# Kernel optimization log

Measured on AMD Instinct MI355X. Metric: run time of the kernel, lower is better.

## Reference

```python
import jax, jax.numpy as jnp
import numpy as np

HEADS = 8

def _conv(x, w, b, stride, pad):
    # x: [B,C,H,W], w: [O,I,kh,kw] (torch OIHW layout)
    y = jax.lax.conv_general_dilated(x, w, (stride, stride), ((pad, pad), (pad, pad)),
                                     dimension_numbers=('NCHW', 'OIHW', 'NCHW'))
    return y + b[None, :, None, None]

def _maxpool2x2(x):
    # returns pooled values and one-hot argmax per 2x2 window (torch first-max tie-break)
    b, c, H, W = x.shape
    win = x.reshape(b, c, H // 2, 2, W // 2, 2).transpose(0, 1, 2, 4, 3, 5).reshape(b, c, H // 2, W // 2, 4)
    am = jnp.argmax(win, axis=-1)
    oh = jax.nn.one_hot(am, 4, dtype=x.dtype)
    pooled = jnp.sum(win * oh, axis=-1)
    return pooled, oh

def _maxunpool2x2(y, oh):
    b, c, h2, w2 = y.shape
    out = y[..., None] * oh  # [b,c,h2,w2,4]
    out = out.reshape(b, c, h2, w2, 2, 2).transpose(0, 1, 2, 4, 3, 5).reshape(b, c, h2 * 2, w2 * 2)
    return out

def _mha2d(x, wq, wk, wv, wo):
    # x: [b,c,h,w]; wq/wk/wv/wo stored as [in,out] so y = x @ W
    b, c, h, w = x.shape
    hw = h * w
    dk = wq.shape[1]
    dh = dk // HEADS
    xt = x.reshape(b, c, hw).transpose(0, 2, 1)  # [b,hw,c]
    def split(y):  # torch: view(b,hw,dh,heads).permute(0,3,1,2)
        return y.reshape(b, hw, dh, HEADS).transpose(0, 3, 1, 2)  # [b,heads,hw,dh]
    q = split(xt @ wq)
    k = split(xt @ wk)
    v = split(xt @ wv)
    scale = jnp.sqrt(jnp.asarray(dh, x.dtype))
    attn = jax.nn.softmax(jnp.einsum('bhqd,bhkd->bhqk', q, k) / scale, axis=-1)
    o = jnp.einsum('bhqk,bhkd->bhqd', attn, v)
    o = o.transpose(0, 2, 3, 1).reshape(b, hw, dk)  # [b,hw,dh,heads] -> merge
    o = o @ wo
    return o.transpose(0, 2, 1).reshape(b, dk, h, w)

def setup_inputs() -> dict:
    key = jax.random.key(0)
    ks = jax.random.split(key, 10)
    B, C, H, W = 16, 256, 64, 64
    s = 0.05
    return {
        'x': jax.random.normal(ks[0], (B, C, H, W), jnp.float32),
        'conv_w': jax.random.normal(ks[1], (C, C, 3, 3), jnp.float32) * s,
        'conv_b': jax.random.normal(ks[2], (C,), jnp.float32) * s,
        'fr_w': jax.random.normal(ks[3], (C, C, 1, 1), jnp.float32) * s,
        'fr_b': jax.random.normal(ks[4], (C,), jnp.float32) * s,
        'wq': jax.random.normal(ks[5], (C, C), jnp.float32) * s,
        'wk': jax.random.normal(ks[6], (C, C), jnp.float32) * s,
        'wv': jax.random.normal(ks[7], (C, C), jnp.float32) * s,
        'wo': jax.random.normal(ks[8], (C, C), jnp.float32) * s,
        'gamma': jax.random.normal(ks[9], (1,), jnp.float32) * 0.1,
    }

def reference(x, conv_w, conv_b, fr_w, fr_b, wq, wk, wv, wo, gamma):
    _x = _conv(x, fr_w, fr_b, 1, 0)          # 1x1 feature reduction
    _x, oh = _maxpool2x2(_x)                 # MaxPool2d(2, return_indices=True)
    _x = _mha2d(_x, wq, wk, wv, wo)          # attention over pooled grid
    _x = _maxunpool2x2(_x, oh)               # MaxUnpool2d(2)
    return _x * jnp.tanh(gamma[0]) + _conv(x, conv_w, conv_b, 1, 1)
```

## Files before the change

### kernel.cpp

```cpp
#include <hip/hip_runtime.h>
#include <hip/hip_bf16.h>
#include <math.h>

#define B 16
#define C 256
#define H 64
#define W 64
#define H2 32
#define W2 32
#define HW2 1024
#define HEADS 8
#define DH 32

typedef unsigned short ushort_t;
using short8 = __attribute__((ext_vector_type(8))) short;
using u16x8  = __attribute__((ext_vector_type(8))) unsigned short;
using f32x4  = __attribute__((ext_vector_type(4))) float;

__device__ inline ushort_t f2bf(float f) {
    __hip_bfloat16 hb = __float2bfloat16(f);
    return *(ushort_t*)&hb;
}
__device__ inline float bf2f(ushort_t u) {
    return __uint_as_float(((unsigned)u) << 16);
}

__device__ __forceinline__ void cp16(const ushort_t* g, ushort_t* l) {
    __builtin_amdgcn_global_load_lds(
        (const __attribute__((address_space(1))) void*)g,
        (__attribute__((address_space(3))) void*)l, 16, 0, 0);
}

#define RSCALE 0.17677669529663687f

__global__ __launch_bounds__(256) void k_prep_wT(const float* __restrict__ cw,
                                                 ushort_t* __restrict__ wbfT) {
    int i = threadIdx.x, o = blockIdx.x;
    const float* src = cw + ((size_t)o * C + i) * 9;
#pragma unroll
    for (int kk = 0; kk < 9; kk++)
        wbfT[((size_t)kk * C + o) * C + i] = f2bf(src[kk]);
}

__global__ __launch_bounds__(256) void k_prep_wx(
    const float* __restrict__ wq, const float* __restrict__ wk,
    const float* __restrict__ wv, const float* __restrict__ wo,
    const float* __restrict__ frw, ushort_t* __restrict__ wqkvT,
    ushort_t* __restrict__ woT, ushort_t* __restrict__ wfr) {
    int op = blockIdx.x, mat = blockIdx.y, t = threadIdx.x;
    if (mat < 3) {
        const float* w = (mat == 0) ? wq : (mat == 1) ? wk : wv;
        int hh = op >> 5, d = op & 31, col = d * 8 + hh;
        wqkvT[(size_t)mat * 65536 + op * 256 + t] = f2bf(w[t * 256 + col]);
    } else if (mat == 3) {
        int hh = t >> 5, d = t & 31, ic = d * 8 + hh;
        woT[op * 256 + t] = f2bf(wo[ic * 256 + op]);
    } else {
        wfr[op * 256 + t] = f2bf(frw[op * 256 + t]);
    }
}

__global__ __launch_bounds__(256) void k_prep_xn(const float* __restrict__ x,
                                                 ushort_t* __restrict__ xn) {
    __shared__ ushort_t ldsT[64 * 258];
    int t = threadIdx.x;
    int hp = blockIdx.x, b = blockIdx.y;
    ushort_t* dst = xn + ((size_t)(b * 66 + hp)) * 66 * 256;

    if (hp == 0 || hp == 65) {
        u16x8 z = (u16x8){0, 0, 0, 0, 0, 0, 0, 0};
        for (int i = t; i < 2112; i += 256) *(u16x8*)(dst + i * 8) = z;
        return;
    }
    const float* xb = x + ((size_t)b * 256) * 4096 + (size_t)(hp - 1) * 64;
    {
        int cq = t >> 6, w = t & 63;
#pragma unroll 8
        for (int it = 0; it < 64; ++it) {
            int c = it * 4 + cq;
            float v = xb[(size_t)c * 4096 + w];
            ldsT[w * 258 + c] = f2bf(v);
        }
    }
    __syncthreads();
    {
        u16x8 z = (u16x8){0, 0, 0, 0, 0, 0, 0, 0};
        if (t < 32) *(u16x8*)(dst + t * 8) = z;
        else if (t < 64) *(u16x8*)(dst + 65 * 256 + (t - 32) * 8) = z;
    }
    {
        int half = t >> 7, cl = t & 127;
#pragma unroll 4
        for (int it = 0; it < 32; ++it) {
            int w = it * 2 + half;
            unsigned v = *(const unsigned*)&ldsT[w * 258 + cl * 2];
            *(unsigned*)(dst + (size_t)(w + 1) * 256 + cl * 2) = v;
        }
    }
}

__global__ __launch_bounds__(256) void k_conv1pool_mfma(
    const ushort_t* __restrict__ xn, const ushort_t* __restrict__ wfr,
    const float* __restrict__ frb, ushort_t* __restrict__ Pbf,
    unsigned char* __restrict__ idx) {
    __shared__ __align__(16) ushort_t sh[32768];
    ushort_t* Als = sh;
    ushort_t* Bls = sh + 8192;
    int t = threadIdx.x;
    int wg = blockIdx.x;
    int mt = (wg & 7) * 64 + (wg >> 3);
    int b = mt >> 5;
    int h0 = (mt * 2) & 63;

    int r = t >> 2, p = t & 3;
    int kswz = (p ^ ((r >> 1) & 3)) * 8;
    const ushort_t* aB0 = xn + ((size_t)((b * 66 + h0 + 1) * 66 + (r + 1))) * 256 + kswz;
    const ushort_t* aB1 = xn + ((size_t)((b * 66 + h0 + 2) * 66 + (r + 1))) * 256 + kswz;
    const ushort_t* bB = wfr + (size_t)r * 256 + kswz;

    f32x4 acc[4][8];
#pragma unroll
    for (int mf = 0; mf < 4; mf++)
#pragma unroll
        for (int nf = 0; nf < 8; nf++) acc[mf][nf] = (f32x4){0.f, 0.f, 0.f, 0.f};

    cp16(aB0, &Als[t * 8]);
    cp16(aB1, &Als[2048 + t * 8]);
    cp16(bB, &Bls[t * 8]);
    cp16(bB + 64 * 256, &Bls[2048 + t * 8]);
    cp16(bB + 128 * 256, &Bls[4096 + t * 8]);
    cp16(bB + 192 * 256, &Bls[6144 + t * 8]);
    __syncthreads();

    int l = t & 63, wid = t >> 6, wm = wid >> 1, wn = wid & 1;
    int arow = wm * 64 + (l & 15);
    int brow = wn * 128 + (l & 15);
    int pslot = ((l >> 4) ^ ((l >> 1) & 3)) * 8;

    for (int s = 0; s < 8; s++) {
        int cur = s & 1;
        if (s < 7) {
            int off = (s + 1) * 32;
            int nb = cur ^ 1;
            cp16(aB0 + off, &Als[nb * 4096 + t * 8]);
            cp16(aB1 + off, &Als[nb * 4096 + 2048 + t * 8]);
            cp16(bB + off, &Bls[nb * 8192 + t * 8]);
            cp16(bB + 64 * 256 + off, &Bls[nb * 8192 + 2048 + t * 8]);
            cp16(bB + 128 * 256 + off, &Bls[nb * 8192 + 4096 + t * 8]);
            cp16(bB + 192 * 256 + off, &Bls[nb * 8192 + 6144 + t * 8]);
        }
        short8 af[4], bf[8];
#pragma unroll
        for (int mf = 0; mf < 4; mf++)
            af[mf] = *(const short8*)&Als[cur * 4096 + (arow + mf * 16) * 32 + pslot];
#pragma unroll
        for (int nf = 0; nf < 8; nf++)
            bf[nf] = *(const short8*)&Bls[cur * 8192 + (brow + nf * 16) * 32 + pslot];
#pragma unroll
        for (int mf = 0; mf < 4; mf++)
#pragma unroll
            for (int nf = 0; nf < 8; nf++)
                acc[mf][nf] = __builtin_amdgcn_mfma_f32_16x16x32_bf16(
                    af[mf], bf[nf], acc[mf][nf], 0, 0, 0);
        __syncthreads();
    }

#pragma unroll
    for (int nf = 0; nf < 8; nf++) {
        int o = wn * 128 + nf * 16 + (l & 15);
        float bias = frb[o];
#pragma unroll
        for (int mf = 0; mf < 4; mf++) {
            int rbase = wm * 64 + mf * 16 + ((l >> 4) << 2);
            f32x4 a = acc[mf][nf];
#pragma unroll
            for (int jj = 0; jj < 4; jj++)
                sh[(rbase + jj) * 256 + o] = f2bf(a[jj] + bias);
        }
    }
    __syncthreads();

    {
        int h2 = mt & 31;
        size_t rowb = (size_t)(b << 10) + h2 * 32;
        int o0 = (t & 31) * 8;
#pragma unroll
        for (int pp = 0; pp < 4; pp++) {
            int w2 = pp * 8 + (t >> 5);
            u16x8 r0 = *(const u16x8*)&sh[(2 * w2) * 256 + o0];
            u16x8 r1 = *(const u16x8*)&sh[(2 * w2 + 1) * 256 + o0];
            u16x8 r2 = *(const u16x8*)&sh[(64 + 2 * w2) * 256 + o0];
            u16x8 r3 = *(const u16x8*)&sh[(64 + 2 * w2 + 1) * 256 + o0];
            u16x8 pv;
            unsigned amlo = 0, amhi = 0;
#pragma unroll
            for (int e = 0; e < 8; e++) {
                float v0 = bf2f(r0[e]), v1 = bf2f(r1[e]);
                float v2 = bf2f(r2[e]), v3 = bf2f(r3[e]);
                float m = v0;
                ushort_t raw = r0[e];
                unsigned am = 0;
                if (v1 > m) { m = v1; raw = r1[e]; am = 1; }
                if (v2 > m) { m = v2; raw = r2[e]; am = 2; }
                if (v3 > m) { m = v3; raw = r3[e]; am = 3; }
                pv[e] = raw;
                if (e < 4) amlo |= am << (8 * e);
                else       amhi |= am << (8 * (e - 4));
            }
            size_t po = (rowb + w2) * 256 + o0;
            *(u16x8*)(Pbf + po) = pv;
            *(uint2*)(idx + po) = make_uint2(amlo, amhi);
        }
    }
}

__global__ __launch_bounds__(256) void k_qkv_mfma(
    const ushort_t* __restrict__ A, const ushort_t* __restrict__ Bw,
    ushort_t* __restrict__ qb, ushort_t* __restrict__ kb,
    ushort_t* __restrict__ vtb) {
    __shared__ __align__(16) ushort_t Als[2][4096];
    __shared__ __align__(16) ushort_t Bls[2][4096];
    int t = threadIdx.x;
    int wg = blockIdx.x;
    int linear = (wg & 7) * 96 + (wg >> 3);
    int mt = linear / 6, nt = linear % 6;

    int r = t >> 2, p = t & 3;
    int kswz = (p ^ ((r >> 1) & 3)) * 8;
    const ushort_t* aB0 = A + ((size_t)(mt * 128 + r)) * 256 + kswz;
    const ushort_t* aB1 = aB0 + (size_t)64 * 256;
    const ushort_t* bB0 = Bw + ((size_t)(nt * 128 + r)) * 256 + kswz;
    const ushort_t* bB1 = bB0 + (size_t)64 * 256;

    f32x4 acc[4][4];
#pragma unroll
    for (int mf = 0; mf < 4; mf++)
#pragma unroll
        for (int nf = 0; nf < 4; nf++) acc[mf][nf] = (f32x4){0.f, 0.f, 0.f, 0.f};

    cp16(aB0, &Als[0][t * 8]);
    cp16(aB1, &Als[0][2048 + t * 8]);
    cp16(bB0, &Bls[0][t * 8]);
    cp16(bB1, &Bls[0][2048 + t * 8]);
    __syncthreads();

    int l = t & 63, wid = t >> 6, wm = wid >> 1, wn = wid & 1;
    int arow = wm * 64 + (l & 15);
    int brow = wn * 64 + (l & 15);
    int pslot = ((l >> 4) ^ ((l >> 1) & 3)) * 8;

    for (int s = 0; s < 8; s++) {
        int cur = s & 1;
        if (s < 7) {
            int off = (s + 1) * 32;
            int nb = cur ^ 1;
            cp16(aB0 + off, &Als[nb][t * 8]);
            cp16(aB1 + off, &Als[nb][2048 + t * 8]);
            cp16(bB0 + off, &Bls[nb][t * 8]);
            cp16(bB1 + off, &Bls[nb][2048 + t * 8]);
        }
        short8 af[4], bf[4];
#pragma unroll
        for (int mf = 0; mf < 4; mf++)
            af[mf] = *(const short8*)&Als[cur][(arow + mf * 16) * 32 + pslot];
#pragma unroll
        for (int nf = 0; nf < 4; nf++)
            bf[nf] = *(const short8*)&Bls[cur][(brow + nf * 16) * 32 + pslot];
#pragma unroll
        for (int mf = 0; mf < 4; mf++)
#pragma unroll
            for (int nf = 0; nf < 4; nf++)
                acc[mf][nf] = __builtin_amdgcn_mfma_f32_16x16x32_bf16(
                    af[mf], bf[nf], acc[mf][nf], 0, 0, 0);
        __syncthreads();
    }

    if (nt < 4) {
        ushort_t* dst = (nt < 2) ? qb : kb;
        float sc = (nt < 2) ? RSCALE : 1.0f;
        int ccb = (nt & 1) * 128 + wn * 64;
#pragma unroll
        for (int nf = 0; nf < 4; nf++) {
            int cc = ccb + nf * 16 + (l & 15);
#pragma unroll
            for (int mf = 0; mf < 4; mf++) {
                int m = mt * 128 + wm * 64 + mf * 16 + ((l >> 4) << 2);
                f32x4 a = acc[mf][nf];
#pragma unroll
                for (int jj = 0; jj < 4; jj++)
                    dst[(size_t)(m + jj) * 256 + cc] = f2bf(a[jj] * sc);
            }
        }
    } else {
#pragma unroll
        for (int nf = 0; nf < 4; nf++) {
            int cc = (nt & 1) * 128 + wn * 64 + nf * 16 + (l & 15);
#pragma unroll
            for (int mf = 0; mf < 4; mf++) {
                int m = mt * 128 + wm * 64 + mf * 16 + ((l >> 4) << 2);
                int b = m >> 10, n0 = m & 1023;
                f32x4 a = acc[mf][nf];
                unsigned u0 = ((unsigned)f2bf(a[1]) << 16) | f2bf(a[0]);
                unsigned u1 = ((unsigned)f2bf(a[3]) << 16) | f2bf(a[2]);
                *(uint2*)&vtb[((size_t)(b * 256 + cc)) * 1024 + n0] =
                    make_uint2(u0, u1);
            }
        }
    }
}

__global__ __launch_bounds__(256) void k_attn_mfma(
    const ushort_t* __restrict__ qb, const ushort_t* __restrict__ kb,
    const ushort_t* __restrict__ vtb, ushort_t* __restrict__ aoT) {
    __shared__ __align__(16) ushort_t Klds[2][2048];
    __shared__ __align__(16) ushort_t Vlds[2][2048];
    __shared__ __align__(16) ushort_t Plds[4][2304];
    __shared__ float rs_lds[128];

    int t = threadIdx.x;
    int bid = blockIdx.x;
    int swz = (bid & 7) * 128 + (bid >> 3);
    int bh = swz >> 3, qt = swz & 7;
    int b = bh >> 3, h = bh & 7;
    int w = t >> 6, l = t & 63, g = l >> 4, li = l & 15;

    size_t qrow = (size_t)(b * 1024 + qt * 128 + w * 32 + li);
    short8 qv0 = *(const short8*)(qb + qrow * 256 + h * 32 + g * 8);
    short8 qv1 = *(const short8*)(qb + (qrow + 16) * 256 + h * 32 + g * 8);

    int sr = t >> 2, sp = t & 3;
    const ushort_t* kg =
        kb + ((size_t)(b * 1024 + sr)) * 256 + h * 32 + ((sp ^ ((sr >> 1) & 3)) * 8);
    int vd = t >> 3, vs = t & 7;
    const ushort_t* vg =
        vtb + ((size_t)(b * 256 + h * 32 + vd)) * 1024 + ((vs ^ (vd & 7)) * 8);

    f32x4 oacc[2][2];
    f32x4 rsv[2];
#pragma unroll
    for (int qf = 0; qf < 2; qf++) {
        rsv[qf] = (f32x4){0.f, 0.f, 0.f, 0.f};
#pragma unroll
        for (int df = 0; df < 2; df++) oacc[qf][df] = (f32x4){0.f, 0.f, 0.f, 0.f};
    }

    cp16(kg, &Klds[0][t * 8]);
    cp16(vg, &Vlds[0][t * 8]);
    __syncthreads();

    ushort_t* Pw = &Plds[w][0];

    for (int c = 0; c < 16; c++) {
        int cur = c & 1;
        if (c < 15) {
            cp16(kg + (size_t)(c + 1) * 64 * 256, &Klds[cur ^ 1][t * 8]);
            cp16(vg + (c + 1) * 64, &Vlds[cur ^ 1][t * 8]);
        }
        short8 ak[4];
#pragma unroll
        for (int kf = 0; kf < 4; kf++)
            ak[kf] = *(const short8*)&Klds[cur][(16 * kf + li) * 32 +
                                               ((g ^ ((l >> 1) & 3)) * 8)];
#pragma unroll
        for (int qf = 0; qf < 2; qf++) {
            short8 qv = qf ? qv1 : qv0;
#pragma unroll
            for (int kf = 0; kf < 4; kf++) {
                f32x4 st = __builtin_amdgcn_mfma_f32_16x16x32_bf16(
                    ak[kf], qv, (f32x4){0.f, 0.f, 0.f, 0.f}, 0, 0, 0);
                float p0 = __expf(st[0]), p1 = __expf(st[1]);
                float p2 = __expf(st[2]), p3 = __expf(st[3]);
                rsv[qf][0] += p0; rsv[qf][1] += p1;
                rsv[qf][2] += p2; rsv[qf][3] += p3;
                unsigned u0, u1;
                asm("v_cvt_pk_bf16_f32 %0, %1, %2" : "=v"(u0) : "v"(p0), "v"(p1));
                asm("v_cvt_pk_bf16_f32 %0, %1, %2" : "=v"(u1) : "v"(p2), "v"(p3));
                *(uint2*)&Pw[(16 * qf + li) * 72 + 16 * kf + 4 * g] =
                    make_uint2(u0, u1);
            }
        }
#pragma unroll
        for (int win = 0; win < 2; win++) {
            short8 pa[2], bv[2];
#pragma unroll
            for (int qf = 0; qf < 2; qf++)
                pa[qf] = *(const short8*)&Pw[(16 * qf + li) * 72 + win * 32 + 8 * g];
#pragma unroll
            for (int df = 0; df < 2; df++)
                bv[df] = *(const short8*)&Vlds[cur][(16 * df + li) * 64 +
                                                    (((win * 4 + g) ^ (l & 7)) * 8)];
#pragma unroll
            for (int qf = 0; qf < 2; qf++)
#pragma unroll
                for (int df = 0; df < 2; df++)
                    oacc[qf][df] = __builtin_amdgcn_mfma_f32_16x16x32_bf16(
                        pa[qf], bv[df], oacc[qf][df], 0, 0, 0);
        }
        __syncthreads();
    }

#pragma unroll
    for (int qf = 0; qf < 2; qf++) {
        float rs = (rsv[qf][0] + rsv[qf][1]) + (rsv[qf][2] + rsv[qf][3]);
        rs += __shfl_xor(rs, 16);
        rs += __shfl_xor(rs, 32);
        if (l < 16) rs_lds[w * 32 + 16 * qf + li] = rs;
    }
    __syncthreads();

#pragma unroll
    for (int qf = 0; qf < 2; qf++) {
        float4 rs4 = *(const float4*)&rs_lds[w * 32 + 16 * qf + 4 * g];
        float inv[4] = {1.f / rs4.x, 1.f / rs4.y, 1.f / rs4.z, 1.f / rs4.w};
#pragma unroll
        for (int df = 0; df < 2; df++) {
            f32x4 a = oacc[qf][df];
#pragma unroll
            for (int r2 = 0; r2 < 4; r2++) {
                size_t row = (size_t)(b * 1024 + qt * 128 + w * 32 + 16 * qf +
                                      4 * g + r2);
                aoT[row * 256 + h * 32 + 16 * df + li] = f2bf(a[r2] * inv[r2]);
            }
        }
    }
}

__global__ __launch_bounds__(256) void k_oproj_mfma(
    const ushort_t* __restrict__ A, const ushort_t* __restrict__ Bw,
    float* __restrict__ y2) {
    __shared__ __align__(16) ushort_t Als[2][4096];
    __shared__ __align__(16) ushort_t Bls[2][4096];
    int t = threadIdx.x;
    int wg = blockIdx.x;
    int linear = (wg & 7) * 32 + (wg >> 3);
    int nt = linear & 1, mt = linear >> 1;

    int r = t >> 2, p = t & 3;
    int kswz = (p ^ ((r >> 1) & 3)) * 8;
    const ushort_t* aB0 = A + ((size_t)(mt * 128 + r)) * 256 + kswz;
    const ushort_t* aB1 = aB0 + (size_t)64 * 256;
    const ushort_t* bB0 = Bw + ((size_t)(nt * 128 + r)) * 256 + kswz;
    const ushort_t* bB1 = bB0 + (size_t)64 * 256;

    f32x4 acc[4][4];
#pragma unroll
    for (int mf = 0; mf < 4; mf++)
#pragma unroll
        for (int nf = 0; nf < 4; nf++) acc[mf][nf] = (f32x4){0.f, 0.f, 0.f, 0.f};

    cp16(aB0, &Als[0][t * 8]);
    cp16(aB1, &Als[0][2048 + t * 8]);
    cp16(bB0, &Bls[0][t * 8]);
    cp16(bB1, &Bls[0][2048 + t * 8]);
    __syncthreads();

    int l = t & 63, wid = t >> 6, wm = wid >> 1, wn = wid & 1;
    int arow = wm * 64 + (l & 15);
    int brow = wn * 64 + (l & 15);
    int pslot = ((l >> 4) ^ ((l >> 1) & 3)) * 8;

    for (int s = 0; s < 8; s++) {
        int cur = s & 1;
        if (s < 7) {
            int off = (s + 1) * 32;
            int nb = cur ^ 1;
            cp16(aB0 + off, &Als[nb][t * 8]);
            cp16(aB1 + off, &Als[nb][2048 + t * 8]);
            cp16(bB0 + off, &Bls[nb][t * 8]);
            cp16(bB1 + off, &Bls[nb][2048 + t * 8]);
        }
        short8 af[4], bf[4];
#pragma unroll
        for (int mf = 0; mf < 4; mf++)
            af[mf] = *(const short8*)&Als[cur][(arow + mf * 16) * 32 + pslot];
#pragma unroll
        for (int nf = 0; nf < 4; nf++)
            bf[nf] = *(const short8*)&Bls[cur][(brow + nf * 16) * 32 + pslot];
#pragma unroll
        for (int mf = 0; mf < 4; mf++)
#pragma unroll
            for (int nf = 0; nf < 4; nf++)
                acc[mf][nf] = __builtin_amdgcn_mfma_f32_16x16x32_bf16(
                    af[mf], bf[nf], acc[mf][nf], 0, 0, 0);
        __syncthreads();
    }

#pragma unroll
    for (int nf = 0; nf < 4; nf++) {
        int cc = nt * 128 + wn * 64 + nf * 16 + (l & 15);
#pragma unroll
        for (int mf = 0; mf < 4; mf++) {
            int m = mt * 128 + wm * 64 + mf * 16 + ((l >> 4) << 2);
            f32x4 a = acc[mf][nf];
#pragma unroll
            for (int jj = 0; jj < 4; jj++)
                y2[(size_t)(m + jj) * 256 + cc] = a[jj];
        }
    }
}

__global__ __launch_bounds__(512) void k_conv3_mfma(
    const ushort_t* __restrict__ xn, const ushort_t* __restrict__ wbfT,
    const float* __restrict__ cb, const float* __restrict__ y2,
    const unsigned char* __restrict__ idx, const float* __restrict__ gamma,
    float* __restrict__ out) {
    extern __shared__ __align__(16) ushort_t lds[];
    ushort_t* AL = lds;
    ushort_t* BL = lds + 32768;
    int t = threadIdx.x;
    int mt = blockIdx.x;

    int srow = t >> 3, sslot = t & 7;
    int kel = (sslot ^ (srow & 7)) * 8;
    const ushort_t* aP[2][2];
    const ushort_t* bP[2][2];
#pragma unroll
    for (int hf = 0; hf < 2; hf++)
#pragma unroll
        for (int j = 0; j < 2; j++) {
            int row = hf * 128 + j * 64 + srow;
            int m = mt * 256 + row;
            int b0 = m >> 12, h0 = (m >> 6) & 63, w0 = m & 63;
            aP[hf][j] = xn + ((size_t)((b0 * 66 + h0) * 66 + w0)) * 256 + kel;
            bP[hf][j] = wbfT + (size_t)row * 256 + kel;
        }

    auto offA = [](int kt) -> int {
        int it = kt / 9, khkw = kt - it * 9;
        int kh = khkw / 3, kw = khkw - kh * 3;
        return (kh * 66 + kw) * 256 + it * 64;
    };
    auto offB = [](int kt) -> int {
        int it = kt / 9, khkw = kt - it * 9;
        return khkw * 65536 + it * 64;
    };
    auto STAGE_A = [&](int bb, int hf, int kt) {
        int o = offA(kt);
        ushort_t* d = AL + bb * 16384 + hf * 8192 + t * 8;
        cp16(aP[hf][0] + o, d);
        cp16(aP[hf][1] + o, d + 4096);
    };
    auto STAGE_B = [&](int bb, int hf, int kt) {
        int o = offB(kt);
        ushort_t* d = BL + bb * 16384 + hf * 8192 + t * 8;
        cp16(bP[hf][0] + o, d);
        cp16(bP[hf][1] + o, d + 4096);
    };

    f32x4 acc[8][4];
#pragma unroll
    for (int mf = 0; mf < 8; mf++)
#pragma unroll
        for (int nf = 0; nf < 4; nf++) acc[mf][nf] = (f32x4){0.f, 0.f, 0.f, 0.f};

    STAGE_A(0, 0, 0); STAGE_A(0, 1, 0); STAGE_B(0, 0, 0); STAGE_B(0, 1, 0);
    asm volatile("s_waitcnt vmcnt(0)" ::: "memory");
    STAGE_B(1, 0, 1); STAGE_B(1, 1, 1);
    __builtin_amdgcn_s_barrier();
    __builtin_amdgcn_sched_barrier(0);

    int l = t & 63, wid = t >> 6, wm = wid >> 2, wn = wid & 3;
    int lr = l & 15, g = l >> 4, l7 = l & 7;
    int abase = wm * 8192;
    int bbase = (wn >> 1) * 8192 + (wn & 1) * 4096;

    for (int kt = 0; kt < 36; kt++) {
        int cur = kt & 1, nxt = cur ^ 1;
        const ushort_t* Ab = AL + cur * 16384 + abase;
        const ushort_t* Bb = BL + cur * 16384 + bbase;
        short8 afA[4][2], afB[4][2], bf0[2][2], bf1[2][2];
#pragma unroll
        for (int mf = 0; mf < 4; mf++)
#pragma unroll
            for (int kk = 0; kk < 2; kk++)
                afA[mf][kk] = *(const short8*)
                    &Ab[(mf * 16 + lr) * 64 + (((kk * 4 + g) ^ l7) * 8)];
#pragma unroll
        for (int nf = 0; nf < 2; nf++)
#pragma unroll
            for (int kk = 0; kk < 2; kk++)
                bf1[nf][kk] = *(const short8*)
                    &Bb[((nf + 2) * 16 + lr) * 64 + (((kk * 4 + g) ^ l7) * 8)];
        if (kt < 35) STAGE_A(nxt, 0, kt + 1);
        __builtin_amdgcn_sched_barrier(0);
        __builtin_amdgcn_s_barrier();
        __builtin_amdgcn_sched_barrier(0);
        __builtin_amdgcn_s_setprio(1);
#pragma unroll
        for (int kk = 0; kk < 2; kk++)
#pragma unroll
            for (int mf = 0; mf < 4; mf++)
#pragma unroll
                for (int nf = 0; nf < 2; nf++)
                    acc[mf][nf + 2] = __builtin_amdgcn_mfma_f32_16x16x32_bf16(
                        afA[mf][kk], bf1[nf][kk], acc[mf][nf + 2], 0, 0, 0);
        __builtin_amdgcn_s_setprio(0);
#pragma unroll
        for (int nf = 0; nf < 2; nf++)
#pragma unroll
            for (int kk = 0; kk < 2; kk++)
                bf0[nf][kk] = *(const short8*)
                    &Bb[(nf * 16 + lr) * 64 + (((kk * 4 + g) ^ l7) * 8)];
        if (kt < 35) STAGE_A(nxt, 1, kt + 1);
        __builtin_amdgcn_sched_barrier(0);
        __builtin_amdgcn_s_barrier();
        __builtin_amdgcn_sched_barrier(0);
        __builtin_amdgcn_s_setprio(1);
#pragma unroll
        for (int kk = 0; kk < 2; kk++)
#pragma unroll
            for (int mf = 0; mf < 4; mf++)
#pragma unroll
                for (int nf = 0; nf < 2; nf++)
                    acc[mf][nf] = __builtin_amdgcn_mfma_f32_16x16x32_bf16(
                        afA[mf][kk], bf0[nf][kk], acc[mf][nf], 0, 0, 0);
        __builtin_amdgcn_s_setprio(0);
#pragma unroll
        for (int mf = 0; mf < 4; mf++)
#pragma unroll
            for (int kk = 0; kk < 2; kk++)
                afB[mf][kk] = *(const short8*)
                    &Ab[((mf + 4) * 16 + lr) * 64 + (((kk * 4 + g) ^ l7) * 8)];
        __builtin_amdgcn_sched_barrier(0);
        __builtin_amdgcn_s_barrier();
        __builtin_amdgcn_sched_barrier(0);
        __builtin_amdgcn_s_setprio(1);
#pragma unroll
        for (int kk = 0; kk < 2; kk++)
#pragma unroll
            for (int mf = 0; mf < 4; mf++)
#pragma unroll
                for (int nf = 0; nf < 2; nf++)
                    acc[mf + 4][nf + 2] = __builtin_amdgcn_mfma_f32_16x16x32_bf16(
                        afB[mf][kk], bf1[nf][kk], acc[mf + 4][nf + 2], 0, 0, 0);
        __builtin_amdgcn_s_setprio(0);
        if (kt < 34) {
            STAGE_B(cur, 0, kt + 2);
            STAGE_B(cur, 1, kt + 2);
            asm volatile("s_waitcnt vmcnt(4)" ::: "memory");
        } else {
            asm volatile("s_waitcnt vmcnt(0)" ::: "memory");
        }
        __builtin_amdgcn_sched_barrier(0);
        __builtin_amdgcn_s_barrier();
        __builtin_amdgcn_sched_barrier(0);
        __builtin_amdgcn_s_setprio(1);
#pragma unroll
        for (int kk = 0; kk < 2; kk++)
#pragma unroll
            for (int mf = 0; mf < 4; mf++)
#pragma unroll
                for (int nf = 0; nf < 2; nf++)
                    acc[mf + 4][nf] = __builtin_amdgcn_mfma_f32_16x16x32_bf16(
                        afB[mf][kk], bf0[nf][kk], acc[mf + 4][nf], 0, 0, 0);
        __builtin_amdgcn_s_setprio(0);
    }

    float tg = tanhf(gamma[0]);
    int mbase = mt * 256 + wm * 128 + (g << 2);
    int obase = wn * 64 + lr;
#pragma unroll
    for (int nf = 0; nf < 4; nf++) {
        int o = obase + nf * 16;
        float bias = cb[o];
#pragma unroll
        for (int mf = 0; mf < 8; mf++) {
            int m = mbase + mf * 16;
            int b = m >> 12, h = (m >> 6) & 63, w0 = m & 63;
            const unsigned char* idr = idx + ((size_t)(b << 10)) * 256;
            const float* y2r = y2 + ((size_t)(b << 10)) * 256;
            f32x4 a = acc[mf][nf];
            float v4[4];
#pragma unroll
            for (int jj = 0; jj < 4; jj++) {
                int wj = w0 + jj;
                int n2 = ((h >> 1) << 5) + (wj >> 1);
                int j2 = ((h & 1) << 1) + (wj & 1);
                float val = a[jj] + bias;
                if (idr[(size_t)n2 * 256 + o] == (unsigned char)j2)
                    val += tg * y2r[(size_t)n2 * 256 + o];
                v4[jj] = val;
            }
            *(float4*)(out + (((size_t)(b * C + o) * H + h) << 6) + w0) =
                make_float4(v4[0], v4[1], v4[2], v4[3]);
        }
    }
}

extern "C" void kernel_launch(void* const* d_in, const int* in_sizes, int n_in,
                              void* d_out, int out_size, void* d_ws, size_t ws_size,
                              hipStream_t stream) {
    const float* x      = (const float*)d_in[0];
    const float* conv_w = (const float*)d_in[1];
    const float* conv_b = (const float*)d_in[2];
    const float* fr_w   = (const float*)d_in[3];
    const float* fr_b   = (const float*)d_in[4];
    const float* wq     = (const float*)d_in[5];
    const float* wk     = (const float*)d_in[6];
    const float* wv     = (const float*)d_in[7];
    const float* wo     = (const float*)d_in[8];
    const float* gamma  = (const float*)d_in[9];
    float* out = (float*)d_out;
    char* ws = (char*)d_ws;

    ushort_t* wbfT  = (ushort_t*)(ws + 0);
    ushort_t* wfrbf = (ushort_t*)(ws + 1179648);
    ushort_t* wqkvT = (ushort_t*)(ws + 1310720);
    ushort_t* woT   = (ushort_t*)(ws + 1703936);
    ushort_t* xn    = (ushort_t*)(ws + 2097152);
    ushort_t* Pbf   = (ushort_t*)(ws + 37781504);
    unsigned char* idx = (unsigned char*)(ws + 46170112);
    ushort_t* qb    = (ushort_t*)(ws + 50364416);
    ushort_t* kb    = (ushort_t*)(ws + 58753024);
    ushort_t* vtb   = (ushort_t*)(ws + 67141632);
    ushort_t* aoT   = (ushort_t*)(ws + 75530240);
    float* y2       = (float*)(ws + 50364416);

    k_prep_wT<<<dim3(C), dim3(256), 0, stream>>>(conv_w, wbfT);
    k_prep_wx<<<dim3(256, 5), dim3(256), 0, stream>>>(wq, wk, wv, wo, fr_w,
                                                      wqkvT, woT, wfrbf);
    k_prep_xn<<<dim3(66, B), dim3(256), 0, stream>>>(x, xn);
    k_conv1pool_mfma<<<dim3(512), dim3(256), 0, stream>>>(xn, wfrbf, fr_b, Pbf, idx);
    k_qkv_mfma<<<dim3(768), dim3(256), 0, stream>>>(Pbf, wqkvT, qb, kb, vtb);
    k_attn_mfma<<<dim3(1024), dim3(256), 0, stream>>>(qb, kb, vtb, aoT);
    k_oproj_mfma<<<dim3(256), dim3(256), 0, stream>>>(aoT, woT, y2);
    (void)hipFuncSetAttribute(reinterpret_cast<const void*>(k_conv3_mfma),
                              hipFuncAttributeMaxDynamicSharedMemorySize, 131072);
    k_conv3_mfma<<<dim3(256), dim3(512), 131072, stream>>>(xn, wbfT, conv_b, y2, idx,
                                                           gamma, out);
    (void)in_sizes; (void)n_in; (void)out_size; (void)ws_size;
}
```

Before: 213.1 us.

## Double-buffer MFMA operand fragments in registers across GEMM sub-phases

Restructures the main conv GEMM loop into ping-pong register fragment sets, so LDS reads for the next quarter-tile are issued while MFMAs run on the current one. The next k-tile's first fragments are prefetched at the end of each iteration. Global-to-LDS staging and waitcnts are reordered to fit, with a full vmcnt(0) wait replacing the partial one. The aim is to hide LDS read latency behind matrix math, at the cost of higher register pressure and a different barrier placement.

Result: slower. 224.6 us (+5.4%).

```diff
diff --git a/kernel.cpp b/kernel.cpp
--- a/kernel.cpp
+++ b/kernel.cpp
@@ -553,107 +553,75 @@
 #pragma unroll
         for (int nf = 0; nf < 4; nf++) acc[mf][nf] = (f32x4){0.f, 0.f, 0.f, 0.f};
 
+    int l = t & 63, wid = t >> 6, wm = wid >> 2, wn = wid & 3;
+    int lr = l & 15, g = l >> 4, l7 = l & 7;
+    int abase = wm * 8192;
+    int bbase = (wn >> 1) * 8192 + (wn & 1) * 4096;
+
+    short8 Xa[4][2], Xb[2][2], Ya[4][2], Yb[2][2];
+
+    auto READF = [&](short8 (&fa)[4][2], short8 (&fb)[2][2],
+                     const ushort_t* Ab, const ushort_t* Bb, int ah, int bh) {
+#pragma unroll
+        for (int mf = 0; mf < 4; mf++)
+#pragma unroll
+            for (int kk = 0; kk < 2; kk++)
+                fa[mf][kk] = *(const short8*)
+                    &Ab[(ah * 64 + mf * 16 + lr) * 64 + (((kk * 4 + g) ^ l7) * 8)];
+#pragma unroll
+        for (int nf = 0; nf < 2; nf++)
+#pragma unroll
+            for (int kk = 0; kk < 2; kk++)
+                fb[nf][kk] = *(const short8*)
+                    &Bb[(bh * 32 + nf * 16 + lr) * 64 + (((kk * 4 + g) ^ l7) * 8)];
+    };
+    auto MFMAQ = [&](short8 (&fa)[4][2], short8 (&fb)[2][2], int mo, int no) {
+        __builtin_amdgcn_s_setprio(1);
+#pragma unroll
+        for (int kk = 0; kk < 2; kk++)
+#pragma unroll
+            for (int mf = 0; mf < 4; mf++)
+#pragma unroll
+                for (int nf = 0; nf < 2; nf++)
+                    acc[mf + mo][nf + no] = __builtin_amdgcn_mfma_f32_16x16x32_bf16(
+                        fa[mf][kk], fb[nf][kk], acc[mf + mo][nf + no], 0, 0, 0);
+        __builtin_amdgcn_s_setprio(0);
+    };
+    auto BARW = [&]() {
+        __builtin_amdgcn_sched_barrier(0);
+        __builtin_amdgcn_s_barrier();
+        __builtin_amdgcn_sched_barrier(0);
+    };
+
     STAGE_A(0, 0, 0); STAGE_A(0, 1, 0); STAGE_B(0, 0, 0); STAGE_B(0, 1, 0);
     asm volatile("s_waitcnt vmcnt(0)" ::: "memory");
     STAGE_B(1, 0, 1); STAGE_B(1, 1, 1);
     __builtin_amdgcn_s_barrier();
-    __builtin_amdgcn_sched_barrier(0);
-
-    int l = t & 63, wid = t >> 6, wm = wid >> 2, wn = wid & 3;
-    int lr = l & 15, g = l >> 4, l7 = l & 7;
-    int abase = wm * 8192;
-    int bbase = (wn >> 1) * 8192 + (wn & 1) * 4096;
+    READF(Xa, Xb, AL + abase, BL + bbase, 0, 0);
 
     for (int kt = 0; kt < 36; kt++) {
         int cur = kt & 1, nxt = cur ^ 1;
-        const ushort_t* Ab = AL + cur * 16384 + abase;
-        const ushort_t* Bb = BL + cur * 16384 + bbase;
-        short8 afA[4][2], afB[4][2], bf0[2][2], bf1[2][2];
-#pragma unroll
-        for (int mf = 0; mf < 4; mf++)
-#pragma unroll
-            for (int kk = 0; kk < 2; kk++)
-                afA[mf][kk] = *(const short8*)
-                    &Ab[(mf * 16 + lr) * 64 + (((kk * 4 + g) ^ l7) * 8)];
-#pragma unroll
-        for (int nf = 0; nf < 2; nf++)
-#pragma unroll
-            for (int kk = 0; kk < 2; kk++)
-                bf1[nf][kk] = *(const short8*)
-                    &Bb[((nf + 2) * 16 + lr) * 64 + (((kk * 4 + g) ^ l7) * 8)];
-        if (kt < 35) STAGE_A(nxt, 0, kt + 1);
-        __builtin_amdgcn_sched_barrier(0);
-        __builtin_amdgcn_s_barrier();
-        __builtin_amdgcn_sched_barrier(0);
-        __builtin_amdgcn_s_setprio(1);
-#pragma unroll
-        for (int kk = 0; kk < 2; kk++)
-#pragma unroll
-            for (int mf = 0; mf < 4; mf++)
-#pragma unroll
-                for (int nf = 0; nf < 2; nf++)
-                    acc[mf][nf + 2] = __builtin_amdgcn_mfma_f32_16x16x32_bf16(
-                        afA[mf][kk], bf1[nf][kk], acc[mf][nf + 2], 0, 0, 0);
-        __builtin_amdgcn_s_setprio(0);
-#pragma unroll
-        for (int nf = 0; nf < 2; nf++)
-#pragma unroll
-            for (int kk = 0; kk < 2; kk++)
-                bf0[nf][kk] = *(const short8*)
-                    &Bb[(nf * 16 + lr) * 64 + (((kk * 4 + g) ^ l7) * 8)];
-        if (kt < 35) STAGE_A(nxt, 1, kt + 1);
-        __builtin_amdgcn_sched_barrier(0);
-        __builtin_amdgcn_s_barrier();
-        __builtin_amdgcn_sched_barrier(0);
-        __builtin_amdgcn_s_setprio(1);
-#pragma unroll
-        for (int kk = 0; kk < 2; kk++)
-#pragma unroll
-            for (int mf = 0; mf < 4; mf++)
-#pragma unroll
-                for (int nf = 0; nf < 2; nf++)
-                    acc[mf][nf] = __builtin_amdgcn_mfma_f32_16x16x32_bf16(
-                        afA[mf][kk], bf0[nf][kk], acc[mf][nf], 0, 0, 0);
-        __builtin_amdgcn_s_setprio(0);
-#pragma unroll
-        for (int mf = 0; mf < 4; mf++)
-#pragma unroll
-            for (int kk = 0; kk < 2; kk++)
-                afB[mf][kk] = *(const short8*)
-                    &Ab[((mf + 4) * 16 + lr) * 64 + (((kk * 4 + g) ^ l7) * 8)];
-        __builtin_amdgcn_sched_barrier(0);
-        __builtin_amdgcn_s_barrier();
-        __builtin_amdgcn_sched_barrier(0);
-        __builtin_amdgcn_s_setprio(1);
-#pragma unroll
-        for (int kk = 0; kk < 2; kk++)
-#pragma unroll
-            for (int mf = 0; mf < 4; mf++)
-#pragma unroll
-                for (int nf = 0; nf < 2; nf++)
-                    acc[mf + 4][nf + 2] = __builtin_amdgcn_mfma_f32_16x16x32_bf16(
-                        afB[mf][kk], bf1[nf][kk], acc[mf + 4][nf + 2], 0, 0, 0);
-        __builtin_amdgcn_s_setprio(0);
-        if (kt < 34) {
-            STAGE_B(cur, 0, kt + 2);
-            STAGE_B(cur, 1, kt + 2);
-            asm volatile("s_waitcnt vmcnt(4)" ::: "memory");
-        } else {
-            asm volatile("s_waitcnt vmcnt(0)" ::: "memory");
-        }
-        __builtin_amdgcn_sched_barrier(0);
-        __builtin_amdgcn_s_barrier();
-        __builtin_amdgcn_sched_barrier(0);
-        __builtin_amdgcn_s_setprio(1);
-#pragma unroll
-        for (int kk = 0; kk < 2; kk++)
-#pragma unroll
-            for (int mf = 0; mf < 4; mf++)
-#pragma unroll
-                for (int nf = 0; nf < 2; nf++)
-                    acc[mf + 4][nf] = __builtin_amdgcn_mfma_f32_16x16x32_bf16(
-                        afB[mf][kk], bf0[nf][kk], acc[mf + 4][nf], 0, 0, 0);
-        __builtin_amdgcn_s_setprio(0);
+        const ushort_t* Ac = AL + cur * 16384 + abase;
+        const ushort_t* Bc = BL + cur * 16384 + bbase;
+        BARW();
+        if (kt < 35) { STAGE_A(nxt, 0, kt + 1); STAGE_A(nxt, 1, kt + 1); }
+        READF(Ya, Yb, Ac, Bc, 0, 1);
+        MFMAQ(Xa, Xb, 0, 0);
+        BARW();
+        READF(Xa, Xb, Ac, Bc, 1, 1);
+        MFMAQ(Ya, Yb, 0, 2);
+        BARW();
+        asm volatile("s_waitcnt vmcnt(0)" ::: "memory");
+        READF(Ya, Yb, Ac, Bc, 1, 0);
+        MFMAQ(Xa, Xb, 4, 2);
+        BARW();
+        if (kt < 34) { STAGE_B(cur, 0, kt + 2); STAGE_B(cur, 1, kt + 2); }
+        if (kt < 35) {
+            const ushort_t* An = AL + nxt * 16384 + abase;
+            const ushort_t* Bn = BL + nxt * 16384 + bbase;
+            READF(Xa, Xb, An, Bn, 0, 0);
+        }
+        MFMAQ(Ya, Yb, 4, 0);
     }
 
     float tg = tanhf(gamma[0]);
```
